# Performance work log

Measured on AMD Instinct MI355X. Metric: run time of the kernel, lower is better.

Reference implementation:

```python
import jax, jax.numpy as jnp
import numpy as np
from jax import lax

# pywt 'db6' rec_lo (scaling filter). dec_lo = rec_lo[::-1]; pytorch_wavelets
# stores dec filters flipped for conv (=correlation), so analysis correlation
# filters are exactly rec_lo and rec_hi = qmf(rec_lo). Synthesis filters for
# conv_transpose are rec_lo/rec_hi unflipped -> same arrays.
_DB6 = np.array([0.11154074335008017, 0.4946238903983854, 0.7511339080215775,
                 0.3152503517092432, -0.22626469396516913, -0.12976686756709563,
                 0.09750160558707936, 0.02752286553001629, -0.031582039318031156,
                 0.0005538422009938016, 0.004777257511010651, -0.00107730108499558],
                dtype=np.float32)
_QMF = (_DB6[::-1].copy() * ((-1.0) ** np.arange(12))).astype(np.float32)
H0, H1 = jnp.asarray(_DB6), jnp.asarray(_QMF)
LF, J = 12, 3
BATCH, SEQ_LEN, CH = 128, 720, 321
COMP_L = [99, 365, 188, 99]   # [yl, yh1, yh2, yh3] for seq_len=720
OUT_L = [22, 57, 34, 22]      # same decomposition of red_len=104


def afb1d(x):
    """One-level analysis filter bank, mode='symmetric'. x: [B,C,N]."""
    B, C, N = x.shape
    out = (N + LF - 1) // 2                      # pywt dwt_coeff_len (symmetric)
    p = 2 * (out - 1) - N + LF
    xp = jnp.pad(x, ((0, 0), (0, 0), (p // 2, (p + 1) // 2)), mode='symmetric')
    w = jnp.stack([H0, H1])[:, None, :]          # [2,1,LF]
    y = lax.conv_general_dilated(xp.reshape(B * C, 1, -1), w, (2,), 'VALID',
                                 dimension_numbers=('NCH', 'OIH', 'NCH'))
    y = y.reshape(B, C, 2, out)
    return y[:, :, 0], y[:, :, 1]


def sfb1d(lo, hi):
    """One-level synthesis bank == conv_transpose1d(stride=2, padding=LF-2)."""
    B, C, Lin = lo.shape
    z = jnp.stack([lo, hi], axis=2).reshape(B * C, 2, Lin)
    w = jnp.stack([H0[::-1], H1[::-1]])[None]    # [1,2,LF], flipped for corr
    y = lax.conv_general_dilated(z, w, (1,), ((1, 1),), lhs_dilation=(2,),
                                 dimension_numbers=('NCH', 'OIH', 'NCH'))
    return y.reshape(B, C, -1)                   # length 2*Lin + 2 - LF


def sinusoidal_pe(n_pos, d):
    pos = jnp.arange(n_pos, dtype=jnp.float32)[:, None]
    div = jnp.exp(jnp.arange(0, d, 2, dtype=jnp.float32) * (-np.log(10000.0) / d))
    pe = jnp.zeros((n_pos, d), jnp.float32)
    pe = pe.at[:, 0::2].set(jnp.sin(pos * div))
    pe = pe.at[:, 1::2].set(jnp.cos(pos * div[: d // 2]))
    return pe


def _forward(x, qws, qbs, kws, kbs, pws, pbs, iws, als, bes):
    mean = lax.stop_gradient(jnp.mean(x, axis=1, keepdims=True))
    std = lax.stop_gradient(jnp.sqrt(jnp.var(x, axis=1, keepdims=True) + 1e-5))
    xc = jnp.transpose((x - mean) / std, (0, 2, 1))      # [B,C,L]
    yl, yh = xc, []
    for _ in range(J):
        yl, hi = afb1d(yl)
        yh.append(hi)
    decomps = [yl] + yh                                  # lengths COMP_L
    preds = []
    for i, comp in enumerate(decomps):
        B, C, L = comp.shape
        Q = jnp.tanh(comp @ qws[i].T + qbs[i])           # [B,C,L]
        K = jnp.tanh(comp @ kws[i].T + kbs[i])
        scores = jnp.einsum('bcl,bcs->bls', Q, K) / (L ** 0.5)
        weighted = jnp.mean(jnp.tanh(scores), axis=1)    # [B,S] (equal per channel)
        cum = jnp.flip(jnp.cumsum(jnp.flip(weighted, -1), -1), -1)
        P = jax.nn.softmax(cum * als[i][0], axis=-1)
        idxs = jnp.arange(L, dtype=jnp.float32)
        win = jnp.sum(P * idxs, axis=-1)[:, None, None]  # soft truncation [B,1,1]
        mask = jax.nn.sigmoid((idxs[None, None, :] - win) * bes[i][0])
        pred = (comp * mask) @ pws[i].T + pbs[i]         # [B,C,O]
        pred = jax.nn.softmax(iws[i], axis=1) * (pred + sinusoidal_pe(C, pred.shape[-1])[None])
        preds.append(pred)
    ll = preds[0]
    for h in preds[:0:-1]:                               # coarsest high band first
        if ll.shape[-1] > h.shape[-1]:
            ll = ll[..., : h.shape[-1]]
        ll = sfb1d(ll, h)
    return ll, mean, std


def setup_inputs() -> dict:
    key = jax.random.key(0)
    ks = jax.random.split(key, 64)
    inp = {'x': jax.random.normal(ks[0], (BATCH, SEQ_LEN, CH), jnp.float32)}
    k = 1
    for i, (L, O) in enumerate(zip(COMP_L, OUT_L)):
        s = 1.0 / np.sqrt(L)                             # torch Linear default init
        inp[f'qw{i}'] = jax.random.uniform(ks[k], (L, L), jnp.float32, -s, s); k += 1
        inp[f'qb{i}'] = jax.random.uniform(ks[k], (L,), jnp.float32, -s, s); k += 1
        inp[f'kw{i}'] = jax.random.uniform(ks[k], (L, L), jnp.float32, -s, s); k += 1
        inp[f'kb{i}'] = jax.random.uniform(ks[k], (L,), jnp.float32, -s, s); k += 1
        inp[f'pw{i}'] = jnp.full((O, L), 1.0 / L, jnp.float32)
        inp[f'pb{i}'] = jnp.zeros((O,), jnp.float32)
        inp[f'iw{i}'] = jnp.ones((1, CH, O), jnp.float32)
        inp[f'al{i}'] = jnp.full((1,), 10.0, jnp.float32)
        inp[f'be{i}'] = jnp.full((1,), 10.0, jnp.float32)
    return inp


def reference(x, qw0, qb0, kw0, kb0, pw0, pb0, iw0, al0, be0,
              qw1, qb1, kw1, kb1, pw1, pb1, iw1, al1, be1,
              qw2, qb2, kw2, kb2, pw2, pb2, iw2, al2, be2,
              qw3, qb3, kw3, kb3, pw3, pb3, iw3, al3, be3):
    return _forward(x, [qw0, qw1, qw2, qw3], [qb0, qb1, qb2, qb3],
                    [kw0, kw1, kw2, kw3], [kb0, kb1, kb2, kb3],
                    [pw0, pw1, pw2, pw3], [pb0, pb1, pb2, pb3],
                    [iw0, iw1, iw2, iw3], [al0, al1, al2, al3],
                    [be0, be1, be2, be3])
```

## Files before the change

kernel.cpp:

```cpp
#include <hip/hip_runtime.h>
#include <hip/hip_bf16.h>
#include <math.h>

namespace {
constexpr int kB  = 128;
constexpr int kC  = 321;
constexpr int kN0 = 720;
constexpr int kCp = 384;
}

typedef __attribute__((ext_vector_type(8))) short short8;
typedef __attribute__((ext_vector_type(4))) float floatx4;

__constant__ float c_h0[12] = {
  0.11154074335008017f, 0.4946238903983854f, 0.7511339080215775f,
  0.3152503517092432f, -0.22626469396516913f, -0.12976686756709563f,
  0.09750160558707936f, 0.02752286553001629f, -0.031582039318031156f,
  0.0005538422009938016f, 0.004777257511010651f, -0.00107730108499558f};
__constant__ float c_h1[12] = {
  -0.00107730108499558f, -0.004777257511010651f, 0.0005538422009938016f,
  0.031582039318031156f, 0.02752286553001629f, -0.09750160558707936f,
  -0.12976686756709563f, 0.22626469396516913f, 0.3152503517092432f,
  -0.7511339080215775f, 0.4946238903983854f, -0.11154074335008017f};
__constant__ float c_h0r[12] = {
  -0.00107730108499558f, 0.004777257511010651f, 0.0005538422009938016f,
  -0.031582039318031156f, 0.02752286553001629f, 0.09750160558707936f,
  -0.12976686756709563f, -0.22626469396516913f, 0.3152503517092432f,
  0.7511339080215775f, 0.4946238903983854f, 0.11154074335008017f};
__constant__ float c_h1r[12] = {
  -0.11154074335008017f, 0.4946238903983854f, -0.7511339080215775f,
  0.3152503517092432f, 0.22626469396516913f, -0.12976686756709563f,
  -0.09750160558707936f, 0.02752286553001629f, 0.031582039318031156f,
  0.0005538422009938016f, -0.004777257511010651f, -0.00107730108499558f};

__device__ __forceinline__ float fast_tanh(float x) {
  float e = __expf(2.f * x);
  return 1.f - 2.f / (e + 1.f);
}
__device__ __forceinline__ unsigned short f2b(float f) {
  __hip_bfloat16 h = __float2bfloat16(f);
  return __builtin_bit_cast(unsigned short, h);
}

__global__ void __launch_bounds__(128) partial_ms_kernel(
    const float* __restrict__ x, float* __restrict__ ps, float* __restrict__ ps2) {
  int b = blockIdx.x, chunk = blockIdx.y;
  int c = blockIdx.z * 128 + threadIdx.x;
  if (c >= kC) return;
  const float* xb = x + (size_t)b * kN0 * kC + c;
  int t0 = chunk * 90;
  float s = 0.f, s2 = 0.f;
#pragma unroll 15
  for (int i = 0; i < 90; ++i) {
    float v = xb[(size_t)(t0 + i) * kC];
    s += v; s2 += v * v;
  }
  ps [(b * 8 + chunk) * kC + c] = s;
  ps2[(b * 8 + chunk) * kC + c] = s2;
}

__global__ void __launch_bounds__(256) finalize_ms_kernel(
    const float* __restrict__ ps, const float* __restrict__ ps2,
    float* __restrict__ mout, float* __restrict__ sout,
    float* __restrict__ meanw, float* __restrict__ invw) {
  int i = blockIdx.x * 256 + threadIdx.x;
  if (i >= kB * kC) return;
  int b = i / kC, c = i - b * kC;
  float s = 0.f, s2 = 0.f;
#pragma unroll
  for (int k = 0; k < 8; ++k) { s += ps[(b * 8 + k) * kC + c]; s2 += ps2[(b * 8 + k) * kC + c]; }
  float mean = s * (1.f / (float)kN0);
  float var = s2 * (1.f / (float)kN0) - mean * mean;
  float sd = sqrtf(var + 1e-5f);
  mout[i] = mean; sout[i] = sd;
  meanw[i] = mean; invw[i] = 1.f / sd;
}

__device__ __forceinline__ int sym_reflect(int t, int N) {
  t = (t < 0) ? (-1 - t) : t;
  t = (t >= N) ? (2 * N - 1 - t) : t;
  return t;
}

template <bool NORM, bool LO_F32, bool LO_BF16>
__global__ void __launch_bounds__(256) dwt_fused_kernel(
    const float* __restrict__ in, const float* __restrict__ meanw,
    const float* __restrict__ invw, float* __restrict__ loF,
    unsigned short* __restrict__ loB, unsigned short* __restrict__ hiB,
    int N, int L, int Lp) {
  __shared__ float xs[138][64];
  __shared__ unsigned short los[64][72];
  __shared__ unsigned short his[64][72];
  const int b = blockIdx.z;
  const int n0 = blockIdx.x * 64, c0 = blockIdx.y * 64;
  const int tid = threadIdx.x;
  const int cl = tid & 63, wv = tid >> 6;
  const int c = c0 + cl;
  const int t0 = 2 * n0 - 10;
  const float* ib = in + (size_t)b * N * kC;
  float mean = 0.f, inv = 1.f;
  if (NORM && c < kC) { mean = meanw[b * kC + c]; inv = invw[b * kC + c]; }
  for (int r = wv; r < 138; r += 4) {
    int t = sym_reflect(t0 + r, N);
    float v = (c < kC) ? ib[(size_t)t * kC + c] : 0.f;
    if (NORM) v = (v - mean) * inv;
    xs[r][cl] = v;
  }
  __syncthreads();
#pragma unroll 4
  for (int k = 0; k < 16; ++k) {
    int nl = wv + 4 * k;
    int n = n0 + nl;
    float a0 = 0.f, a1 = 0.f;
    int base = 2 * nl;
#pragma unroll
    for (int j = 0; j < 12; ++j) {
      float v = xs[base + j][cl];
      a0 += v * c_h0[j]; a1 += v * c_h1[j];
    }
    bool valid = (n < L) && (c < kC);
    if (LO_F32 && valid) loF[((size_t)b * L + n) * kC + c] = a0;
    if (LO_BF16) los[cl][nl] = f2b(valid ? a0 : 0.f);
    his[cl][nl] = f2b(valid ? a1 : 0.f);
  }
  __syncthreads();
  int row = tid >> 2, part = tid & 3;
  size_t dst = ((size_t)b * kCp + c0 + row) * Lp + n0 + part * 16;
  *(uint4*)(hiB + dst)     = *(const uint4*)&his[row][part * 16];
  *(uint4*)(hiB + dst + 8) = *(const uint4*)&his[row][part * 16 + 8];
  if (LO_BF16) {
    *(uint4*)(loB + dst)     = *(const uint4*)&los[row][part * 16];
    *(uint4*)(loB + dst + 8) = *(const uint4*)&los[row][part * 16 + 8];
  }
}

struct WcArgs { const float* src[8]; unsigned short* dst[8]; int L[8]; int Lp[8]; };
__global__ void __launch_bounds__(256) wconv_all_kernel(WcArgs a) {
  int lvl = blockIdx.y;
  int Lp = a.Lp[lvl], L = a.L[lvl];
  int i = blockIdx.x * 256 + threadIdx.x;
  if (i >= Lp * Lp) return;
  int p = i / Lp, l = i - p * Lp;
  a.dst[lvl][i] = f2b((p < L && l < L) ? a.src[lvl][(size_t)p * L + l] : 0.f);
}

struct QKAllArgs {
  const unsigned short* W[8];
  const unsigned short* Xt[4];
  const float* bias[8];
  unsigned short* Y[8];
  int Lp[4], L[4], yOff[4];
};
__global__ void __launch_bounds__(256) qk_all_kernel(QKAllArgs a) {
  const int y = blockIdx.y;
  const int lvl = (y >= a.yOff[1]) + (y >= a.yOff[2]) + (y >= a.yOff[3]);
  const int Lp = a.Lp[lvl], L = a.L[lvl];
  const int rel = y - a.yOff[lvl];
  const int pt = Lp >> 7;
  const int sel = rel / pt;
  const int pBase = (rel - sel * pt) * 128;
  const unsigned short* Wb = a.W[2 * lvl + sel] + (size_t)pBase * Lp;
  const float* bias = a.bias[2 * lvl + sel];
  unsigned short* Yd = a.Y[2 * lvl + sel];
  const int b = blockIdx.z;
  const int cBase = blockIdx.x * 128;
  const int tid = threadIdx.x;
  const int ln = tid & 63, w = tid >> 6;
  const int wm = w & 1, wn = w >> 1;
  __shared__ short As[128 * 72];
  __shared__ short Bs[128 * 72];
  floatx4 acc[4][4] = {};
  const unsigned short* Xb = a.Xt[lvl] + ((size_t)b * kCp + cBase) * Lp;
  const int kIters = Lp >> 6;
  for (int kt = 0; kt < kIters; ++kt) {
    const int lc = kt << 6;
#pragma unroll
    for (int q = 0; q < 4; ++q) {
      int id = q * 256 + tid;
      int row = id >> 3, pos = (id & 7) * 8;
      *(uint4*)&As[row * 72 + pos] = *(const uint4*)(Wb + (size_t)row * Lp + lc + pos);
      *(uint4*)&Bs[row * 72 + pos] = *(const uint4*)(Xb + (size_t)row * Lp + lc + pos);
    }
    __syncthreads();
#pragma unroll
    for (int sub = 0; sub < 2; ++sub) {
      short8 av[4], bv[4];
#pragma unroll
      for (int mi = 0; mi < 4; ++mi)
        av[mi] = *(const short8*)&As[(wm * 64 + mi * 16 + (ln & 15)) * 72 + (ln >> 4) * 8 + sub * 32];
#pragma unroll
      for (int ni = 0; ni < 4; ++ni)
        bv[ni] = *(const short8*)&Bs[(wn * 64 + ni * 16 + (ln & 15)) * 72 + (ln >> 4) * 8 + sub * 32];
#pragma unroll
      for (int mi = 0; mi < 4; ++mi)
#pragma unroll
        for (int ni = 0; ni < 4; ++ni)
          acc[mi][ni] = __builtin_amdgcn_mfma_f32_16x16x32_bf16(av[mi], bv[ni], acc[mi][ni], 0, 0, 0);
    }
    __syncthreads();
  }
#pragma unroll
  for (int mi = 0; mi < 4; ++mi) {
#pragma unroll
    for (int r = 0; r < 4; ++r) {
      int p = pBase + wm * 64 + mi * 16 + (ln >> 4) * 4 + r;
      float bv = (p < L) ? bias[p] : 0.f;
#pragma unroll
      for (int ni = 0; ni < 4; ++ni) {
        int c = cBase + wn * 64 + ni * 16 + (ln & 15);
        float v = (p < L && c < kC) ? fast_tanh(acc[mi][ni][r] + bv) : 0.f;
        Yd[((size_t)b * Lp + p) * kCp + c] = f2b(v);
      }
    }
  }
}

struct ScAllArgs {
  const unsigned short* Q[4]; const unsigned short* K[4];
  float* wgt[4];
  int Lp[4], L[4], tOff[4];
  float scale[4];
};
__global__ void __launch_bounds__(256) scores_all_kernel(ScAllArgs a) {
  const int t = blockIdx.x;
  const int lvl = (t >= a.tOff[1]) + (t >= a.tOff[2]) + (t >= a.tOff[3]);
  const int rel = t - a.tOff[lvl];
  const int Lp = a.Lp[lvl], L = a.L[lvl];
  const int pt = Lp >> 7;
  const int sBase = (rel % pt) * 128;
  const int lBase = (rel / pt) * 128;
  const int b = blockIdx.y;
  const int tid = threadIdx.x;
  const int ln = tid & 63, w = tid >> 6;
  const int wm = w & 1, wn = w >> 1;
  __shared__ short As[128 * 72];
  __shared__ short Bs[128 * 72];
  __shared__ float red[128];
  floatx4 acc[4][4] = {};
  const unsigned short* Qp = a.Q[lvl] + ((size_t)b * Lp + lBase) * kCp;
  const unsigned short* Kp = a.K[lvl] + ((size_t)b * Lp + sBase) * kCp;
  for (int cc = 0; cc < kCp; cc += 64) {
#pragma unroll
    for (int q = 0; q < 4; ++q) {
      int id = q * 256 + tid;
      int row = id >> 3, pos = (id & 7) * 8;
      *(uint4*)&As[row * 72 + pos] = *(const uint4*)(Qp + (size_t)row * kCp + cc + pos);
      *(uint4*)&Bs[row * 72 + pos] = *(const uint4*)(Kp + (size_t)row * kCp + cc + pos);
    }
    __syncthreads();
#pragma unroll
    for (int sub = 0; sub < 2; ++sub) {
      short8 av[4], bv[4];
#pragma unroll
      for (int mi = 0; mi < 4; ++mi)
        av[mi] = *(const short8*)&As[(wm * 64 + mi * 16 + (ln & 15)) * 72 + (ln >> 4) * 8 + sub * 32];
#pragma unroll
      for (int ni = 0; ni < 4; ++ni)
        bv[ni] = *(const short8*)&Bs[(wn * 64 + ni * 16 + (ln & 15)) * 72 + (ln >> 4) * 8 + sub * 32];
#pragma unroll
      for (int mi = 0; mi < 4; ++mi)
#pragma unroll
        for (int ni = 0; ni < 4; ++ni)
          acc[mi][ni] = __builtin_amdgcn_mfma_f32_16x16x32_bf16(av[mi], bv[ni], acc[mi][ni], 0, 0, 0);
    }
    __syncthreads();
  }
  if (tid < 128) red[tid] = 0.f;
  __syncthreads();
  const float scale = a.scale[lvl];
#pragma unroll
  for (int ni = 0; ni < 4; ++ni) {
    float p = 0.f;
#pragma unroll
    for (int mi = 0; mi < 4; ++mi)
#pragma unroll
      for (int r = 0; r < 4; ++r) p += fast_tanh(acc[mi][ni][r] * scale);
    p += __shfl_xor(p, 16);
    p += __shfl_xor(p, 32);
    if ((ln & 48) == 0) atomicAdd(&red[wn * 64 + ni * 16 + (ln & 15)], p);
  }
  __syncthreads();
  if (tid < 128) {
    int s = sBase + tid;
    if (s < L) atomicAdd(&a.wgt[lvl][(size_t)b * L + s], red[tid]);
  }
}

struct WinArgs { const float* wgt[4]; const float* al[4]; const float* be[4];
                 float* mask[4]; int L[4]; };
__global__ void __launch_bounds__(64) winmask_all_kernel(WinArgs a) {
  int lvl = blockIdx.y;
  int b = blockIdx.x, lane = threadIdx.x;
  int L = a.L[lvl];
  const float* wgt = a.wgt[lvl] + (size_t)b * L;
  float al = a.al[lvl][0], be = a.be[lvl][0];
  float invL = 1.f / (float)L;
  int chunk = (L + 63) >> 6;
  int s0 = lane * chunk;
  float v[6];
  float csum = 0.f;
  for (int i = chunk - 1; i >= 0; --i) {
    int s = s0 + i;
    float xv = (s < L) ? wgt[s] * invL : 0.f;
    csum += xv; v[i] = csum;
  }
  float tot = csum;
  for (int o = 1; o < 64; o <<= 1) {
    float t = __shfl_down(tot, o);
    if (lane + o < 64) tot += t;
  }
  float excl = tot - csum;
  float m = -1e30f;
  for (int i = 0; i < chunk; ++i)
    if (s0 + i < L) m = fmaxf(m, al * (v[i] + excl));
  for (int o = 32; o; o >>= 1) m = fmaxf(m, __shfl_xor(m, o));
  float sum = 0.f, num = 0.f;
  for (int i = 0; i < chunk; ++i) {
    int s = s0 + i;
    if (s < L) { float e = __expf(al * (v[i] + excl) - m); sum += e; num += e * (float)s; }
  }
  for (int o = 32; o; o >>= 1) { sum += __shfl_xor(sum, o); num += __shfl_xor(num, o); }
  float win = num / sum;
  float* mk = a.mask[lvl] + (size_t)b * L;
  for (int i = 0; i < chunk; ++i) {
    int s = s0 + i;
    if (s < L) mk[s] = 1.f / (1.f + __expf(-((float)s - win) * be));
  }
}

struct IwArgs { const float* iw[4]; float* sm[4]; int O[4]; };
__global__ void __launch_bounds__(64) iwsm_all_kernel(IwArgs a) {
  int x = blockIdx.x;
  int lvl, o;
  if (x < 22) { lvl = 0; o = x; }
  else if (x < 79) { lvl = 1; o = x - 22; }
  else if (x < 113) { lvl = 2; o = x - 79; }
  else { lvl = 3; o = x - 113; }
  int O = a.O[lvl];
  const float* iw = a.iw[lvl];
  int lane = threadIdx.x;
  float m = -1e30f;
  for (int c = lane; c < kC; c += 64) m = fmaxf(m, iw[c * O + o]);
  for (int k = 32; k; k >>= 1) m = fmaxf(m, __shfl_xor(m, k));
  float sum = 0.f;
  for (int c = lane; c < kC; c += 64) sum += __expf(iw[c * O + o] - m);
  for (int k = 32; k; k >>= 1) sum += __shfl_xor(sum, k);
  float inv = 1.f / sum;
  for (int c = lane; c < kC; c += 64) a.sm[lvl][c * O + o] = __expf(iw[c * O + o] - m) * inv;
}

struct PredAllArgs {
  const unsigned short* Xt[4];
  const float* PW[4]; const float* PB[4]; const float* MK[4]; const float* SM[4];
  float* OUT[4];
  int L[4], Lp[4], O[4];
};
__global__ void __launch_bounds__(256) pred_all_kernel(PredAllArgs a) {
  const int lvl = blockIdx.y;
  const int L = a.L[lvl], Lp = a.Lp[lvl], O = a.O[lvl];
  const float* PW = a.PW[lvl];
  const int b = blockIdx.z;
  const int cBase = blockIdx.x * 128;
  const int tid = threadIdx.x;
  const int ln = tid & 63, w = tid >> 6;
  __shared__ short As[64 * 40];
  __shared__ short Bs[128 * 40];
  floatx4 acc[8] = {};
  const unsigned short* Xb = a.Xt[lvl] + ((size_t)b * kCp + cBase) * Lp;
  const float* mk = a.MK[lvl] + (size_t)b * L;
  for (int lc = 0; lc < Lp; lc += 32) {
    {
      int o = tid >> 2, j0 = (tid & 3) * 8;
      alignas(16) unsigned short tmp[8];
#pragma unroll
      for (int j = 0; j < 8; ++j) {
        int l = lc + j0 + j;
        float v = (o < O && l < L) ? PW[(size_t)o * L + l] * mk[l] : 0.f;
        tmp[j] = f2b(v);
      }
      *(uint4*)&As[o * 40 + j0] = *(const uint4*)tmp;
    }
#pragma unroll
    for (int q = 0; q < 2; ++q) {
      int ch = tid * 2 + q;
      int row = ch >> 2, pos = ch & 3;
      *(uint4*)(&Bs[row * 40 + pos * 8]) = *(const uint4*)(Xb + (size_t)row * Lp + lc + pos * 8);
    }
    __syncthreads();
    short8 av = *(const short8*)&As[(w * 16 + (ln & 15)) * 40 + (ln >> 4) * 8];
#pragma unroll
    for (int ni = 0; ni < 8; ++ni) {
      short8 bb = *(const short8*)&Bs[(ni * 16 + (ln & 15)) * 40 + (ln >> 4) * 8];
      acc[ni] = __builtin_amdgcn_mfma_f32_16x16x32_bf16(av, bb, acc[ni], 0, 0, 0);
    }
    __syncthreads();
  }
  const float negln = -logf(10000.f) / (float)O;
#pragma unroll
  for (int ni = 0; ni < 8; ++ni) {
    int c = cBase + ni * 16 + (ln & 15);
    if (c >= kC) continue;
#pragma unroll
    for (int r = 0; r < 4; ++r) {
      int o = w * 16 + (ln >> 4) * 4 + r;
      if (o >= O) continue;
      float dv = __expf(negln * (float)(2 * (o >> 1)));
      float ang = (float)c * dv;
      float pe = (o & 1) ? cosf(ang) : sinf(ang);
      a.OUT[lvl][((size_t)b * O + o) * kC + c] = a.SM[lvl][c * O + o] * (acc[ni][r] + a.PB[lvl][o] + pe);
    }
  }
}

__global__ void __launch_bounds__(256) sfb_fused_kernel(
    const float* __restrict__ P0, const float* __restrict__ P1,
    const float* __restrict__ P2, const float* __restrict__ P3,
    float* __restrict__ out) {
  __shared__ float p0s[22][32], p3s[22][32], p2s[34][32], p1s[57][32];
  __shared__ float r1s[34][32], r2s[58][32];
  __shared__ float outs[104][33];
  int b = blockIdx.y, c0 = blockIdx.x * 32;
  int tid = threadIdx.x;
  int cl = tid & 31, r = tid >> 5;
  int c = c0 + cl;
  bool cv = c < kC;
  for (int o = r; o < 22; o += 8) {
    p0s[o][cl] = cv ? P0[((size_t)b * 22 + o) * kC + c] : 0.f;
    p3s[o][cl] = cv ? P3[((size_t)b * 22 + o) * kC + c] : 0.f;
  }
  for (int o = r; o < 34; o += 8) p2s[o][cl] = cv ? P2[((size_t)b * 34 + o) * kC + c] : 0.f;
  for (int o = r; o < 57; o += 8) p1s[o][cl] = cv ? P1[((size_t)b * 57 + o) * kC + c] : 0.f;
  __syncthreads();
  for (int n = r; n < 34; n += 8) {
    float acc = 0.f;
#pragma unroll
    for (int j = 0; j < 12; ++j) {
      int m = n + j - 1;
      if (m < 0 || (m & 1)) continue;
      int i = m >> 1;
      if (i >= 22) continue;
      acc += c_h0r[j] * p0s[i][cl] + c_h1r[j] * p3s[i][cl];
    }
    r1s[n][cl] = acc;
  }
  __syncthreads();
  for (int n = r; n < 58; n += 8) {
    float acc = 0.f;
#pragma unroll
    for (int j = 0; j < 12; ++j) {
      int m = n + j - 1;
      if (m < 0 || (m & 1)) continue;
      int i = m >> 1;
      if (i >= 34) continue;
      acc += c_h0r[j] * r1s[i][cl] + c_h1r[j] * p2s[i][cl];
    }
    r2s[n][cl] = acc;
  }
  __syncthreads();
  for (int n = r; n < 104; n += 8) {
    float acc = 0.f;
#pragma unroll
    for (int j = 0; j < 12; ++j) {
      int m = n + j - 1;
      if (m < 0 || (m & 1)) continue;
      int i = m >> 1;
      if (i >= 57) continue;
      acc += c_h0r[j] * r2s[i][cl] + c_h1r[j] * p1s[i][cl];
    }
    outs[n][cl] = acc;
  }
  __syncthreads();
  for (int idx = tid; idx < 32 * 104; idx += 256) {
    int ci = idx / 104, n = idx - ci * 104;
    int cg = c0 + ci;
    if (cg < kC) out[((size_t)b * kC + cg) * 104 + n] = outs[n][ci];
  }
}

extern "C" void kernel_launch(void* const* d_in, const int* in_sizes, int n_in,
                              void* d_out, int out_size, void* d_ws, size_t ws_size,
                              hipStream_t stream) {
  (void)in_sizes; (void)n_in; (void)out_size; (void)ws_size;
  const float* x = (const float*)d_in[0];
  auto inp = [&](int lvl, int j) { return (const float*)d_in[1 + 9 * lvl + j]; };

  float* outf = (float*)d_out;
  float* mout = outf + (size_t)kB * kC * 104;
  float* sout = mout + (size_t)kB * kC;

  float* Wp = (float*)d_ws;
  size_t off = 0;
  auto alloc = [&](size_t n) { float* p = Wp + off; off += (n + 63) & ~(size_t)63; return p; };

  float* LO1 = alloc((size_t)kB * 365 * kC);
  float* LO2 = alloc((size_t)kB * 188 * kC);
  unsigned short* Xt1 = (unsigned short*)alloc((size_t)kB * kCp * 384 / 2);
  unsigned short* Xt2 = (unsigned short*)alloc((size_t)kB * kCp * 256 / 2);
  unsigned short* Xt0 = (unsigned short*)alloc((size_t)kB * kCp * 128 / 2);
  unsigned short* Xt3 = (unsigned short*)alloc((size_t)kB * kCp * 128 / 2);
  unsigned short* KbfAll = (unsigned short*)alloc((size_t)kB * kCp * 896 / 2);
  unsigned short* Wpv[8];
  for (int i = 0; i < 8; ++i)
    Wpv[i] = (unsigned short*)alloc((size_t)384 * 384 / 2);
  float* wgtAll = alloc((size_t)kB * (99 + 365 + 188 + 99));
  float* M0 = alloc((size_t)kB * 99);  float* M1 = alloc((size_t)kB * 365);
  float* M2 = alloc((size_t)kB * 188); float* M3 = alloc((size_t)kB * 99);
  float* S0 = alloc((size_t)kC * 22);  float* S1 = alloc((size_t)kC * 57);
  float* S2 = alloc((size_t)kC * 34);  float* S3 = alloc((size_t)kC * 22);
  float* P0 = alloc((size_t)kB * 22 * kC); float* P1 = alloc((size_t)kB * 57 * kC);
  float* P2 = alloc((size_t)kB * 34 * kC); float* P3 = alloc((size_t)kB * 22 * kC);
  float* ps   = alloc((size_t)kB * 8 * kC);
  float* ps2  = alloc((size_t)kB * 8 * kC);
  float* meanw = alloc((size_t)kB * kC);
  float* invw  = alloc((size_t)kB * kC);
  unsigned short* QbfAll = (unsigned short*)LO1;

  const int Lc[4]  = {99, 365, 188, 99};
  const int Lpv[4] = {128, 384, 256, 128};
  const int Ov[4]  = {22, 57, 34, 22};
  const int prefLp[4] = {0, 128, 512, 768};
  const int wOff[4] = {0, 99, 99 + 365, 99 + 365 + 188};
  unsigned short* Qlvl[4]; unsigned short* Klvl[4];
  for (int i = 0; i < 4; ++i) {
    Qlvl[i] = QbfAll + (size_t)kB * kCp * prefLp[i];
    Klvl[i] = KbfAll + (size_t)kB * kCp * prefLp[i];
  }
  const unsigned short* Xts[4] = {Xt0, Xt1, Xt2, Xt3};
  float* masks[4] = {M0, M1, M2, M3};
  float* smws[4]  = {S0, S1, S2, S3};
  float* preds[4] = {P0, P1, P2, P3};

  partial_ms_kernel<<<dim3(kB, 8, 3), 128, 0, stream>>>(x, ps, ps2);
  finalize_ms_kernel<<<(kB * kC + 255) / 256, 256, 0, stream>>>(ps, ps2, mout, sout, meanw, invw);

  dwt_fused_kernel<true, true, false><<<dim3(6, kCp / 64, kB), 256, 0, stream>>>(
      x, meanw, invw, LO1, nullptr, Xt1, kN0, 365, 384);
  dwt_fused_kernel<false, true, false><<<dim3(4, kCp / 64, kB), 256, 0, stream>>>(
      LO1, nullptr, nullptr, LO2, nullptr, Xt2, 365, 188, 256);
  dwt_fused_kernel<false, false, true><<<dim3(2, kCp / 64, kB), 256, 0, stream>>>(
      LO2, nullptr, nullptr, nullptr, Xt0, Xt3, 188, 99, 128);

  {
    WcArgs wa;
    for (int i = 0; i < 4; ++i) {
      wa.src[2 * i] = inp(i, 0); wa.src[2 * i + 1] = inp(i, 2);
      wa.dst[2 * i] = Wpv[2 * i]; wa.dst[2 * i + 1] = Wpv[2 * i + 1];
      wa.L[2 * i] = wa.L[2 * i + 1] = Lc[i];
      wa.Lp[2 * i] = wa.Lp[2 * i + 1] = Lpv[i];
    }
    wconv_all_kernel<<<dim3(576, 8), 256, 0, stream>>>(wa);
  }
  hipMemsetAsync(wgtAll, 0, (size_t)kB * (99 + 365 + 188 + 99) * sizeof(float), stream);

  {
    QKAllArgs qa;
    for (int i = 0; i < 4; ++i) {
      qa.W[2 * i] = Wpv[2 * i]; qa.W[2 * i + 1] = Wpv[2 * i + 1];
      qa.bias[2 * i] = inp(i, 1); qa.bias[2 * i + 1] = inp(i, 3);
      qa.Y[2 * i] = Qlvl[i]; qa.Y[2 * i + 1] = Klvl[i];
      qa.Xt[i] = Xts[i]; qa.Lp[i] = Lpv[i]; qa.L[i] = Lc[i];
    }
    qa.yOff[0] = 0; qa.yOff[1] = 2; qa.yOff[2] = 8; qa.yOff[3] = 12;
    qk_all_kernel<<<dim3(kCp / 128, 14, kB), 256, 0, stream>>>(qa);
  }

  {
    ScAllArgs sa;
    for (int i = 0; i < 4; ++i) {
      sa.Q[i] = Qlvl[i]; sa.K[i] = Klvl[i];
      sa.wgt[i] = wgtAll + (size_t)kB * wOff[i];
      sa.Lp[i] = Lpv[i]; sa.L[i] = Lc[i];
      sa.scale[i] = 1.0f / sqrtf((float)Lc[i]);
    }
    sa.tOff[0] = 0; sa.tOff[1] = 1; sa.tOff[2] = 10; sa.tOff[3] = 14;
    scores_all_kernel<<<dim3(15, kB), 256, 0, stream>>>(sa);
  }

  {
    WinArgs wa;
    for (int i = 0; i < 4; ++i) {
      wa.wgt[i] = wgtAll + (size_t)kB * wOff[i];
      wa.al[i] = inp(i, 7); wa.be[i] = inp(i, 8);
      wa.mask[i] = masks[i]; wa.L[i] = Lc[i];
    }
    winmask_all_kernel<<<dim3(kB, 4), 64, 0, stream>>>(wa);
    IwArgs ia;
    for (int i = 0; i < 4; ++i) { ia.iw[i] = inp(i, 6); ia.sm[i] = smws[i]; ia.O[i] = Ov[i]; }
    iwsm_all_kernel<<<135, 64, 0, stream>>>(ia);
  }

  {
    PredAllArgs pa;
    for (int i = 0; i < 4; ++i) {
      pa.Xt[i] = Xts[i]; pa.PW[i] = inp(i, 4); pa.PB[i] = inp(i, 5);
      pa.MK[i] = masks[i]; pa.SM[i] = smws[i]; pa.OUT[i] = preds[i];
      pa.L[i] = Lc[i]; pa.Lp[i] = Lpv[i]; pa.O[i] = Ov[i];
    }
    pred_all_kernel<<<dim3(kCp / 128, 4, kB), 256, 0, stream>>>(pa);
  }

  sfb_fused_kernel<<<dim3(11, kB), 256, 0, stream>>>(P0, P1, P2, P3, outf);
}
```

Measured before the change: 843.7 us.

## Register-prefetch next K tile, XOR-swizzle LDS, and stage QK output through LDS

Both the QK projection and scores GEMM kernels now load the next 64-wide K slice into registers while MFMAs run on the current slice, so global latency overlaps compute. The padded 72-stride LDS layout becomes a 64-stride XOR-swizzled layout to avoid bank conflicts at lower shared-memory use. The QK kernel also writes its tanh output into LDS first, then does coalesced 16-byte stores instead of scattered 2-byte global stores. The cost is more registers per thread, which could reduce occupancy.

Result: slower. 1.120 ms (+32.7%).

```diff
diff --git a/kernel.cpp b/kernel.cpp
--- a/kernel.cpp
+++ b/kernel.cpp
@@ -167,30 +167,52 @@
   const int tid = threadIdx.x;
   const int ln = tid & 63, w = tid >> 6;
   const int wm = w & 1, wn = w >> 1;
-  __shared__ short As[128 * 72];
-  __shared__ short Bs[128 * 72];
+  __shared__ alignas(16) short smem[16384];
+  short* As = smem;
+  short* Bs = smem + 8192;
   floatx4 acc[4][4] = {};
   const unsigned short* Xb = a.Xt[lvl] + ((size_t)b * kCp + cBase) * Lp;
   const int kIters = Lp >> 6;
+  const int r0 = tid >> 3, g = tid & 7;
+  const int sw = (g ^ (r0 & 7)) * 8;
+  uint4 ra[4], rb[4];
+#pragma unroll
+  for (int q = 0; q < 4; ++q) {
+    size_t go = (size_t)(q * 32 + r0) * Lp + g * 8;
+    ra[q] = *(const uint4*)(Wb + go);
+    rb[q] = *(const uint4*)(Xb + go);
+  }
   for (int kt = 0; kt < kIters; ++kt) {
-    const int lc = kt << 6;
 #pragma unroll
     for (int q = 0; q < 4; ++q) {
-      int id = q * 256 + tid;
-      int row = id >> 3, pos = (id & 7) * 8;
-      *(uint4*)&As[row * 72 + pos] = *(const uint4*)(Wb + (size_t)row * Lp + lc + pos);
-      *(uint4*)&Bs[row * 72 + pos] = *(const uint4*)(Xb + (size_t)row * Lp + lc + pos);
+      *(uint4*)&As[(q * 32 + r0) * 64 + sw] = ra[q];
+      *(uint4*)&Bs[(q * 32 + r0) * 64 + sw] = rb[q];
     }
     __syncthreads();
+    if (kt + 1 < kIters) {
+      int lc = (kt + 1) << 6;
+#pragma unroll
+      for (int q = 0; q < 4; ++q) {
+        size_t go = (size_t)(q * 32 + r0) * Lp + lc + g * 8;
+        ra[q] = *(const uint4*)(Wb + go);
+        rb[q] = *(const uint4*)(Xb + go);
+      }
+    }
 #pragma unroll
     for (int sub = 0; sub < 2; ++sub) {
       short8 av[4], bv[4];
 #pragma unroll
-      for (int mi = 0; mi < 4; ++mi)
-        av[mi] = *(const short8*)&As[(wm * 64 + mi * 16 + (ln & 15)) * 72 + (ln >> 4) * 8 + sub * 32];
-#pragma unroll
-      for (int ni = 0; ni < 4; ++ni)
-        bv[ni] = *(const short8*)&Bs[(wn * 64 + ni * 16 + (ln & 15)) * 72 + (ln >> 4) * 8 + sub * 32];
+      for (int mi = 0; mi < 4; ++mi) {
+        int row = wm * 64 + mi * 16 + (ln & 15);
+        int col = (ln >> 4) * 8 + sub * 32;
+        av[mi] = *(const short8*)&As[row * 64 + (col ^ ((row & 7) * 8))];
+      }
+#pragma unroll
+      for (int ni = 0; ni < 4; ++ni) {
+        int row = wn * 64 + ni * 16 + (ln & 15);
+        int col = (ln >> 4) * 8 + sub * 32;
+        bv[ni] = *(const short8*)&Bs[row * 64 + (col ^ ((row & 7) * 8))];
+      }
 #pragma unroll
       for (int mi = 0; mi < 4; ++mi)
 #pragma unroll
@@ -199,19 +221,32 @@
     }
     __syncthreads();
   }
+  short* Ys = smem;
 #pragma unroll
   for (int mi = 0; mi < 4; ++mi) {
 #pragma unroll
     for (int r = 0; r < 4; ++r) {
-      int p = pBase + wm * 64 + mi * 16 + (ln >> 4) * 4 + r;
-      float bv = (p < L) ? bias[p] : 0.f;
+      int prow = wm * 64 + mi * 16 + (ln >> 4) * 4 + r;
+      int p = pBase + prow;
+      float bvv = (p < L) ? bias[p] : 0.f;
+      int f = ((prow >> 2) & 3) * 32;
 #pragma unroll
       for (int ni = 0; ni < 4; ++ni) {
-        int c = cBase + wn * 64 + ni * 16 + (ln & 15);
-        float v = (p < L && c < kC) ? fast_tanh(acc[mi][ni][r] + bv) : 0.f;
-        Yd[((size_t)b * Lp + p) * kCp + c] = f2b(v);
-      }
-    }
+        int ccol = wn * 64 + ni * 16 + (ln & 15);
+        int c = cBase + ccol;
+        float v = (p < L && c < kC) ? fast_tanh(acc[mi][ni][r] + bvv) : 0.f;
+        Ys[prow * 128 + (ccol ^ f)] = (short)f2b(v);
+      }
+    }
+  }
+  __syncthreads();
+  unsigned short* Yrow = Yd + ((size_t)b * Lp + pBase) * kCp + cBase;
+#pragma unroll
+  for (int t = 0; t < 8; ++t) {
+    int id = t * 256 + tid;
+    int row = id >> 4, cg = (id & 15) * 8;
+    int csw = cg ^ (((row >> 2) & 3) * 32);
+    *(uint4*)(Yrow + (size_t)row * kCp + cg) = *(const uint4*)&Ys[row * 128 + csw];
   }
 }
 
@@ -233,30 +268,53 @@
   const int tid = threadIdx.x;
   const int ln = tid & 63, w = tid >> 6;
   const int wm = w & 1, wn = w >> 1;
-  __shared__ short As[128 * 72];
-  __shared__ short Bs[128 * 72];
+  __shared__ alignas(16) short smem[16384];
+  short* As = smem;
+  short* Bs = smem + 8192;
   __shared__ float red[128];
   floatx4 acc[4][4] = {};
   const unsigned short* Qp = a.Q[lvl] + ((size_t)b * Lp + lBase) * kCp;
   const unsigned short* Kp = a.K[lvl] + ((size_t)b * Lp + sBase) * kCp;
-  for (int cc = 0; cc < kCp; cc += 64) {
+  const int r0 = tid >> 3, g = tid & 7;
+  const int sw = (g ^ (r0 & 7)) * 8;
+  uint4 ra[4], rb[4];
+#pragma unroll
+  for (int q = 0; q < 4; ++q) {
+    size_t go = (size_t)(q * 32 + r0) * kCp + g * 8;
+    ra[q] = *(const uint4*)(Qp + go);
+    rb[q] = *(const uint4*)(Kp + go);
+  }
+  for (int kt = 0; kt < kCp / 64; ++kt) {
 #pragma unroll
     for (int q = 0; q < 4; ++q) {
-      int id = q * 256 + tid;
-      int row = id >> 3, pos = (id & 7) * 8;
-      *(uint4*)&As[row * 72 + pos] = *(const uint4*)(Qp + (size_t)row * kCp + cc + pos);
-      *(uint4*)&Bs[row * 72 + pos] = *(const uint4*)(Kp + (size_t)row * kCp + cc + pos);
+      *(uint4*)&As[(q * 32 + r0) * 64 + sw] = ra[q];
+      *(uint4*)&Bs[(q * 32 + r0) * 64 + sw] = rb[q];
     }
     __syncthreads();
+    if (kt + 1 < kCp / 64) {
+      int cc = (kt + 1) << 6;
+#pragma unroll
+      for (int q = 0; q < 4; ++q) {
+        size_t go = (size_t)(q * 32 + r0) * kCp + cc + g * 8;
+        ra[q] = *(const uint4*)(Qp + go);
+        rb[q] = *(const uint4*)(Kp + go);
+      }
+    }
 #pragma unroll
     for (int sub = 0; sub < 2; ++sub) {
       short8 av[4], bv[4];
 #pragma unroll
-      for (int mi = 0; mi < 4; ++mi)
-        av[mi] = *(const short8*)&As[(wm * 64 + mi * 16 + (ln & 15)) * 72 + (ln >> 4) * 8 + sub * 32];
-#pragma unroll
-      for (int ni = 0; ni < 4; ++ni)
-        bv[ni] = *(const short8*)&Bs[(wn * 64 + ni * 16 + (ln & 15)) * 72 + (ln >> 4) * 8 + sub * 32];
+      for (int mi = 0; mi < 4; ++mi) {
+        int row = wm * 64 + mi * 16 + (ln & 15);
+        int col = (ln >> 4) * 8 + sub * 32;
+        av[mi] = *(const short8*)&As[row * 64 + (col ^ ((row & 7) * 8))];
+      }
+#pragma unroll
+      for (int ni = 0; ni < 4; ++ni) {
+        int row = wn * 64 + ni * 16 + (ln & 15);
+        int col = (ln >> 4) * 8 + sub * 32;
+        bv[ni] = *(const short8*)&Bs[row * 64 + (col ^ ((row & 7) * 8))];
+      }
 #pragma unroll
       for (int mi = 0; mi < 4; ++mi)
 #pragma unroll
```
